# Optimization experiments

Measured on AMD Instinct MI355X. Metric: run time of the kernel, lower is better.

The kernel has to match this reference:

```python
import jax, jax.numpy as jnp
import numpy as np

N_HEADS = 16
HEAD_SIZE = 64
EMBED = 1024
BLOCK = 2048
B, T = 2, 2048


def setup_inputs() -> dict:
    key = jax.random.key(0)
    ks = jax.random.split(key, 6)
    scale = 0.02
    inputs = jax.random.normal(ks[0], (B, T, EMBED), dtype=jnp.float32)
    # per-head projection weights, stacked: [H, E, D]
    Wk = jax.random.normal(ks[1], (N_HEADS, EMBED, HEAD_SIZE), dtype=jnp.float32) * scale
    Wq = jax.random.normal(ks[2], (N_HEADS, EMBED, HEAD_SIZE), dtype=jnp.float32) * scale
    Wv = jax.random.normal(ks[3], (N_HEADS, EMBED, HEAD_SIZE), dtype=jnp.float32) * scale
    Wo = jax.random.normal(ks[4], (EMBED, EMBED), dtype=jnp.float32) * scale
    bo = jax.random.normal(ks[5], (EMBED,), dtype=jnp.float32) * scale
    return {"inputs": inputs, "Wk": Wk, "Wq": Wq, "Wv": Wv, "Wo": Wo, "bo": bo}


def reference(inputs, Wk, Wq, Wv, Wo, bo):
    # per-head projections: [B,H,T,D]
    k = jnp.einsum("bte,hed->bhtd", inputs, Wk)
    q = jnp.einsum("bte,hed->bhtd", inputs, Wq)
    v = jnp.einsum("bte,hed->bhtd", inputs, Wv)
    # NOTE: original computes wei = K @ Q^T (faithful reproduction)
    wei = jnp.einsum("bhtd,bhsd->bhts", k, q) * (HEAD_SIZE ** -0.5)
    causal = jnp.tril(jnp.ones((T, T), dtype=bool))  # tril==0 masked
    wei = jnp.where(causal, wei, -jnp.inf)
    wei = jax.nn.softmax(wei, axis=-1)
    out = jnp.einsum("bhts,bhsd->bhtd", wei, v)
    # concat heads along feature dim: [B,T,H*D]
    z = out.transpose(0, 2, 1, 3).reshape(B, T, N_HEADS * HEAD_SIZE)
    z = z @ Wo.T + bo  # match torch Linear(x) = x @ W^T + b
    return z
```

## Files before the change

kernel.cpp:

```cpp
#include <hip/hip_runtime.h>
#include <cstdint>
#include <cstddef>

typedef __bf16 bf8_t __attribute__((ext_vector_type(8)));
typedef float  f4_t  __attribute__((ext_vector_type(4)));

static __device__ __forceinline__ f4_t mfma16(bf8_t a, bf8_t b, f4_t c) {
    return __builtin_amdgcn_mfma_f32_16x16x32_bf16(a, b, c, 0, 0, 0);
}

#if defined(__has_builtin) && __has_builtin(__builtin_amdgcn_exp2f)
#define EXP2F(x) __builtin_amdgcn_exp2f(x)
#else
#define EXP2F(x) exp2f(x)
#endif

static __device__ __forceinline__ void async_ld16(const __bf16* g, __bf16* l) {
    __builtin_amdgcn_global_load_lds(
        (const __attribute__((address_space(1))) void*)(uintptr_t)g,
        (__attribute__((address_space(3))) void*)(uintptr_t)l, 16, 0, 0);
}


__global__ void __launch_bounds__(256) prep_all(const float* __restrict__ X,
                                                const float* __restrict__ Wo,
                                                const float* __restrict__ Wq,
                                                const float* __restrict__ Wk,
                                                const float* __restrict__ Wv,
                                                __bf16* __restrict__ Xbf,
                                                __bf16* __restrict__ Wobf,
                                                __bf16* __restrict__ Wqt,
                                                __bf16* __restrict__ Wkt,
                                                __bf16* __restrict__ Wvt) {
    __shared__ float tile[64][65];
    int bx = (int)blockIdx.x;
    if (bx < 2560) {
        const float* src; __bf16* dst; size_t base;
        if (bx < 2048) { src = X;  dst = Xbf;  base = (size_t)bx * 2048; }
        else           { src = Wo; dst = Wobf; base = (size_t)(bx - 2048) * 2048; }
        size_t i = base + (size_t)threadIdx.x * 8;
        float4 a = *(const float4*)(src + i);
        float4 b = *(const float4*)(src + i + 4);
        bf8_t o;
        o[0] = (__bf16)a.x; o[1] = (__bf16)a.y; o[2] = (__bf16)a.z; o[3] = (__bf16)a.w;
        o[4] = (__bf16)b.x; o[5] = (__bf16)b.y; o[6] = (__bf16)b.z; o[7] = (__bf16)b.w;
        *(bf8_t*)(dst + i) = o;
        return;
    }
    int wt = bx - 2560;
    int which = wt >> 8, inner = wt & 255;
    const float* W; __bf16* Wt;
    if (which == 0)      { W = Wq; Wt = Wqt; }
    else if (which == 1) { W = Wk; Wt = Wkt; }
    else                 { W = Wv; Wt = Wvt; }
    int h = inner >> 4, eb = inner & 15;
    int tx = threadIdx.x;
    int e = tx >> 2, dg = (tx & 3) * 16;
    const float* src = W + ((size_t)h * 1024 + eb * 64 + e) * 64 + dg;
#pragma unroll
    for (int i = 0; i < 4; ++i) {
        float4 v = *(const float4*)(src + i * 4);
        tile[dg + i * 4 + 0][e] = v.x;
        tile[dg + i * 4 + 1][e] = v.y;
        tile[dg + i * 4 + 2][e] = v.z;
        tile[dg + i * 4 + 3][e] = v.w;
    }
    __syncthreads();
    int d = tx >> 2, eg = (tx & 3) * 16;
    __bf16* dst = Wt + (size_t)(h * 64 + d) * 1024 + eb * 64 + eg;
    bf8_t o0, o1;
#pragma unroll
    for (int i = 0; i < 8; ++i) o0[i] = (__bf16)tile[d][eg + i];
#pragma unroll
    for (int i = 0; i < 8; ++i) o1[i] = (__bf16)tile[d][eg + 8 + i];
    *(bf8_t*)dst       = o0;
    *(bf8_t*)(dst + 8) = o1;
}

static __device__ __forceinline__ void gemm_tile128(const __bf16* __restrict__ A,
                                                    const __bf16* __restrict__ Bt,
                                                    __bf16* As, __bf16* Bs,
                                                    int m0, int n0, f4_t acc[4][4]) {
    const int tid  = threadIdx.x;
    const int lane = tid & 63;
    const int wv   = tid >> 6;
    const int lrow = lane >> 3;
    const int lsc  = lane & 7;
    const int quad = lane >> 4;
    const int l15  = lane & 15;
    const int wm = (wv & 1) * 64;
    const int wn = (wv >> 1) * 64;
    f4_t zero = {0.f, 0.f, 0.f, 0.f};
#pragma unroll
    for (int mi = 0; mi < 4; ++mi)
#pragma unroll
        for (int ni = 0; ni < 4; ++ni) acc[mi][ni] = zero;

    for (int kb = 0; kb < 16; ++kb) {
#pragma unroll
        for (int j = 0; j < 4; ++j) {
            int row = wv * 32 + j * 8 + lrow;
            int lc  = lsc ^ (row & 7);
            async_ld16(A + (size_t)(m0 + row) * 1024 + kb * 64 + lc * 8,
                       As + (wv * 32 + j * 8) * 64);
            async_ld16(Bt + (size_t)(n0 + row) * 1024 + kb * 64 + lc * 8,
                       Bs + (wv * 32 + j * 8) * 64);
        }
        __syncthreads();
#pragma unroll
        for (int ks = 0; ks < 2; ++ks) {
            bf8_t af[4], bfr[4];
#pragma unroll
            for (int mi = 0; mi < 4; ++mi) {
                int row = wm + mi * 16 + l15;
                int ch  = (ks * 4 + quad) ^ (row & 7);
                af[mi] = *(const bf8_t*)(As + row * 64 + ch * 8);
            }
#pragma unroll
            for (int ni = 0; ni < 4; ++ni) {
                int row = wn + ni * 16 + l15;
                int ch  = (ks * 4 + quad) ^ (row & 7);
                bfr[ni] = *(const bf8_t*)(Bs + row * 64 + ch * 8);
            }
#pragma unroll
            for (int mi = 0; mi < 4; ++mi)
#pragma unroll
                for (int ni = 0; ni < 4; ++ni)
                    acc[mi][ni] = mfma16(af[mi], bfr[ni], acc[mi][ni]);
        }
        __syncthreads();
    }
}

__global__ void __launch_bounds__(256, 3) gemm_proj(const __bf16* __restrict__ Xbf,
                                                    const __bf16* __restrict__ Wqt,
                                                    const __bf16* __restrict__ Wkt,
                                                    const __bf16* __restrict__ Wvt,
                                                    __bf16* __restrict__ Qb,
                                                    __bf16* __restrict__ Kb,
                                                    __bf16* __restrict__ Vt) {
    __shared__ __bf16 smem[17408];
    __bf16* As = smem;
    __bf16* Bs = smem + 8192;
    int which = blockIdx.y;
    const __bf16* Bt = which == 0 ? Wqt : (which == 1 ? Wkt : Wvt);
    int m0 = ((int)blockIdx.x >> 3) * 128;
    int n0 = ((int)blockIdx.x & 7) * 128;
    f4_t acc[4][4];
    gemm_tile128(Xbf, Bt, As, Bs, m0, n0, acc);
    const int lane = threadIdx.x & 63, wv = threadIdx.x >> 6;
    const int quad = lane >> 4, l15 = lane & 15;
    const int wm = (wv & 1) * 64, wn = (wv >> 1) * 64;
    const int STR = 136;
    if (which < 2) {
        __bf16* C = which ? Kb : Qb;
        const float scl = which ? 0.18033688f : 1.0f;
#pragma unroll
        for (int mi = 0; mi < 4; ++mi)
#pragma unroll
            for (int ni = 0; ni < 4; ++ni)
#pragma unroll
                for (int r = 0; r < 4; ++r) {
                    int ml = wm + mi * 16 + quad * 4 + r;
                    int nl = wn + ni * 16 + l15;
                    smem[ml * STR + nl] = (__bf16)(acc[mi][ni][r] * scl);
                }
        __syncthreads();
        int row = (int)threadIdx.x >> 1;
        int seg = (int)threadIdx.x & 1;
        int m = m0 + row;
        int b = m >> 11, t = m & 2047;
        int h = (n0 >> 6) + seg;
        __bf16* dst = C + ((size_t)(b * 16 + h) * 2048 + t) * 64;
        const __bf16* srcl = smem + row * STR + seg * 64;
#pragma unroll
        for (int k = 0; k < 8; ++k)
            *(bf8_t*)(dst + k * 8) = *(const bf8_t*)(srcl + k * 8);
    } else {
#pragma unroll
        for (int mi = 0; mi < 4; ++mi)
#pragma unroll
            for (int ni = 0; ni < 4; ++ni)
#pragma unroll
                for (int r = 0; r < 4; ++r) {
                    int ml = wm + mi * 16 + quad * 4 + r;
                    int nl = wn + ni * 16 + l15;
                    smem[nl * STR + ml] = (__bf16)acc[mi][ni][r];
                }
        __syncthreads();
        int b = m0 >> 11, tg0 = m0 & 2047;
        int nl = (int)threadIdx.x >> 1;
        int tc = ((int)threadIdx.x & 1) * 64;
        int n = n0 + nl, h = n >> 6, d = n & 63;
        __bf16* dst = Vt + ((size_t)(b * 16 + h) * 64 + d) * 2048 + tg0 + tc;
        const __bf16* srcl = smem + nl * STR + tc;
#pragma unroll
        for (int k = 0; k < 8; ++k)
            *(bf8_t*)(dst + k * 8) = *(const bf8_t*)(srcl + k * 8);
    }
}

static __device__ __forceinline__ void gemm_tile(const __bf16* __restrict__ A,
                                                 const __bf16* __restrict__ Bt,
                                                 __bf16* As, __bf16* Bs,
                                                 int m0, int n0, f4_t acc[4][2]) {
    const int tid  = threadIdx.x;
    const int lane = tid & 63;
    const int wv   = tid >> 6;
    const int lrow = lane >> 3;
    const int lsc  = lane & 7;
    const int quad = lane >> 4;
    const int l15  = lane & 15;
    const int wm = (wv & 1) * 64;
    const int wn = (wv >> 1) * 32;
    f4_t zero = {0.f, 0.f, 0.f, 0.f};
#pragma unroll
    for (int mi = 0; mi < 4; ++mi)
#pragma unroll
        for (int ni = 0; ni < 2; ++ni) acc[mi][ni] = zero;

    for (int kb = 0; kb < 16; ++kb) {
#pragma unroll
        for (int j = 0; j < 4; ++j) {
            int row = wv * 32 + j * 8 + lrow;
            int lc  = lsc ^ (row & 7);
            async_ld16(A + (size_t)(m0 + row) * 1024 + kb * 64 + lc * 8,
                       As + (wv * 32 + j * 8) * 64);
        }
#pragma unroll
        for (int j = 0; j < 2; ++j) {
            int row = wv * 16 + j * 8 + lrow;
            int lc  = lsc ^ (row & 7);
            async_ld16(Bt + (size_t)(n0 + row) * 1024 + kb * 64 + lc * 8,
                       Bs + (wv * 16 + j * 8) * 64);
        }
        __syncthreads();
#pragma unroll
        for (int ks = 0; ks < 2; ++ks) {
            bf8_t af[4], bfr[2];
#pragma unroll
            for (int mi = 0; mi < 4; ++mi) {
                int row = wm + mi * 16 + l15;
                int ch  = (ks * 4 + quad) ^ (row & 7);
                af[mi] = *(const bf8_t*)(As + row * 64 + ch * 8);
            }
#pragma unroll
            for (int ni = 0; ni < 2; ++ni) {
                int row = wn + ni * 16 + l15;
                int ch  = (ks * 4 + quad) ^ (row & 7);
                bfr[ni] = *(const bf8_t*)(Bs + row * 64 + ch * 8);
            }
#pragma unroll
            for (int mi = 0; mi < 4; ++mi)
#pragma unroll
                for (int ni = 0; ni < 2; ++ni)
                    acc[mi][ni] = mfma16(af[mi], bfr[ni], acc[mi][ni]);
        }
        __syncthreads();
    }
}

__global__ void __launch_bounds__(256) gemm_out(const __bf16* __restrict__ Ob,
                                                const __bf16* __restrict__ Wobf,
                                                const float* __restrict__ bo,
                                                float* __restrict__ out) {
    __shared__ __bf16 smem[128 * 64 + 64 * 64];
    __bf16* As = smem;
    __bf16* Bs = smem + 128 * 64;
    int m0 = ((int)blockIdx.x >> 4) * 128;
    int n0 = ((int)blockIdx.x & 15) * 64;
    f4_t acc[4][2];
    gemm_tile(Ob, Wobf, As, Bs, m0, n0, acc);
    const int lane = threadIdx.x & 63, wv = threadIdx.x >> 6;
    const int quad = lane >> 4, l15 = lane & 15;
    const int wm = (wv & 1) * 64, wn = (wv >> 1) * 32;
#pragma unroll
    for (int mi = 0; mi < 4; ++mi)
#pragma unroll
        for (int ni = 0; ni < 2; ++ni)
#pragma unroll
            for (int r = 0; r < 4; ++r) {
                int m = m0 + wm + mi * 16 + quad * 4 + r;
                int n = n0 + wn + ni * 16 + l15;
                out[(size_t)m * 1024 + n] = acc[mi][ni][r] + bo[n];
            }
}

__global__ void __launch_bounds__(256, 3) attn(const __bf16* __restrict__ Kb,
                                               const __bf16* __restrict__ Qb,
                                               const __bf16* __restrict__ Vt,
                                               __bf16* __restrict__ Ob,
                                               int* __restrict__ ctrs) {
    __shared__ __bf16 Qs[2][64 * 64];
    __shared__ __bf16 Vs[2][64 * 64];
    __shared__ __bf16 Ps[4][16 * 72];
    __shared__ int item_lds;
    const int tid = threadIdx.x, lane = tid & 63, wv = tid >> 6;
    const int quad = lane >> 4, l15 = lane & 15;
    const int lrow8 = lane >> 3, lchunk = lane & 7;
    int xcc;
    asm volatile("s_getreg_b32 %0, hwreg(HW_REG_XCC_ID)" : "=s"(xcc));
    xcc &= 7;
    int* ctr = ctrs + xcc * 16;
    __bf16* Psw = &Ps[wv][0];
    f4_t zero = {0.f, 0.f, 0.f, 0.f};

    for (;;) {
        if (tid == 0) item_lds = atomicAdd(ctr, 1);
        __syncthreads();
        const int q = item_lds;
        if (q >= 128) break;
        const int tt = 31 - (q >> 2);
        const int bh = xcc * 4 + (q & 3);
        const int b = bh >> 4, h = bh & 15;
        const int t0 = tt * 64;
        const int tw = t0 + wv * 16;
        const __bf16* Kp = Kb + (size_t)bh * 2048 * 64;
        const __bf16* Qp = Qb + (size_t)bh * 2048 * 64;
        const __bf16* Vp = Vt + (size_t)bh * 64 * 2048;

        bf8_t kfrag[2];
#pragma unroll
        for (int ks = 0; ks < 2; ++ks)
            kfrag[ks] = *(const bf8_t*)(Kp + (size_t)(tw + l15) * 64 + ks * 32 + quad * 8);

        f4_t oacc[4];
#pragma unroll
        for (int ni = 0; ni < 4; ++ni) oacc[ni] = zero;
        float lsum[4] = {0.f, 0.f, 0.f, 0.f};

        auto stage = [&](int buf, int s0) {
#pragma unroll
            for (int j = 0; j < 2; ++j) {
                int row = wv * 8 + j * 32 + lrow8;
                int cg  = lchunk ^ (row & 7);
                async_ld16(Qp + (size_t)(s0 + row) * 64 + cg * 8,
                           &Qs[buf][(wv * 8 + j * 32) * 64]);
                async_ld16(Vp + (size_t)row * 2048 + s0 + cg * 8,
                           &Vs[buf][(wv * 8 + j * 32) * 64]);
            }
        };

        const int nsb = tt + 1;
        stage(0, 0);
        for (int sb = 0; sb < nsb; ++sb) {
            const int cur = sb & 1;
            const int s0 = sb * 64;
            const bool masked = (sb == nsb - 1);
            __syncthreads();
            if (sb + 1 < nsb) stage(1 ^ cur, s0 + 64);
            const __bf16* Qc = &Qs[cur][0];
            const __bf16* Vc = &Vs[cur][0];
            f4_t sacc[4] = {zero, zero, zero, zero};
#pragma unroll
            for (int ks = 0; ks < 2; ++ks) {
                bf8_t qf[4];
#pragma unroll
                for (int st = 0; st < 4; ++st) {
                    int row = st * 16 + l15;
                    int ch  = (ks * 4 + quad) ^ (row & 7);
                    qf[st] = *(const bf8_t*)(Qc + row * 64 + ch * 8);
                }
#pragma unroll
                for (int st = 0; st < 4; ++st)
                    sacc[st] = mfma16(kfrag[ks], qf[st], sacc[st]);
            }
#pragma unroll
            for (int st = 0; st < 4; ++st)
#pragma unroll
                for (int r = 0; r < 4; ++r) {
                    float e = EXP2F(sacc[st][r]);
                    if (masked && (s0 + st * 16 + l15 > tw + quad * 4 + r)) e = 0.0f;
                    lsum[r] += e;
                    Psw[(quad * 4 + r) * 72 + st * 16 + l15] = (__bf16)e;
                }
            asm volatile("s_waitcnt lgkmcnt(0)" ::: "memory");
            bf8_t pf[2];
#pragma unroll
            for (int ks = 0; ks < 2; ++ks)
                pf[ks] = *(const bf8_t*)(Psw + l15 * 72 + ks * 32 + quad * 8);
#pragma unroll
            for (int ks = 0; ks < 2; ++ks) {
                bf8_t vf[4];
#pragma unroll
                for (int ni = 0; ni < 4; ++ni) {
                    int row = ni * 16 + l15;
                    int ch  = (ks * 4 + quad) ^ (row & 7);
                    vf[ni] = *(const bf8_t*)(Vc + row * 64 + ch * 8);
                }
#pragma unroll
                for (int ni = 0; ni < 4; ++ni)
                    oacc[ni] = mfma16(pf[ks], vf[ni], oacc[ni]);
            }
        }

#pragma unroll
        for (int r = 0; r < 4; ++r) {
            float l = lsum[r];
            l += __shfl_xor(l, 1);
            l += __shfl_xor(l, 2);
            l += __shfl_xor(l, 4);
            l += __shfl_xor(l, 8);
            float inv = 1.0f / l;
            int t = tw + quad * 4 + r;
#pragma unroll
            for (int ni = 0; ni < 4; ++ni)
                Ob[((size_t)(b * 2048 + t) * 16 + h) * 64 + ni * 16 + l15] =
                    (__bf16)(oacc[ni][r] * inv);
        }
    }
}

extern "C" void kernel_launch(void* const* d_in, const int* in_sizes, int n_in,
                              void* d_out, int out_size, void* d_ws, size_t ws_size,
                              hipStream_t stream) {
    const float* X  = (const float*)d_in[0];
    const float* Wk = (const float*)d_in[1];
    const float* Wq = (const float*)d_in[2];
    const float* Wv = (const float*)d_in[3];
    const float* Wo = (const float*)d_in[4];
    const float* bo = (const float*)d_in[5];
    float* out = (float*)d_out;

    __bf16* ws   = (__bf16*)d_ws;
    __bf16* Xbf  = ws;
    __bf16* Wqt  = ws + 4194304;
    __bf16* Wkt  = ws + 5242880;
    __bf16* Wvt  = ws + 6291456;
    __bf16* Wobf = ws + 7340032;
    __bf16* Qb   = ws + 8388608;
    __bf16* Kb   = ws + 12582912;
    __bf16* Vt   = ws + 16777216;
    __bf16* Ob   = ws + 20971520;
    int* ctrs = (int*)d_ws;

    prep_all<<<3328, 256, 0, stream>>>(X, Wo, Wq, Wk, Wv, Xbf, Wobf, Wqt, Wkt, Wvt);
    gemm_proj<<<dim3(256, 3), 256, 0, stream>>>(Xbf, Wqt, Wkt, Wvt, Qb, Kb, Vt);
    hipMemsetAsync(ctrs, 0, 512, stream);
    attn<<<768, 256, 0, stream>>>(Kb, Qb, Vt, Ob, ctrs);
    gemm_out<<<512, 256, 0, stream>>>(Ob, Wobf, bo, out);
}
```

Before: 174.7 us.

## Keep attention P in registers via lane permutes, raise occupancy, drop memset

The attention kernel swaps the QK MFMA operand order so the S tile comes out transposed, then builds the PV A-operand in registers using permlane32 swaps and xor shuffles instead of writing P to LDS and reading it back. This removes the per-wave P shared buffer and the LDS round trip, and collapses the row-sum to one scalar per lane. Launch bounds rise to 4 blocks per CU with 1024 persistent blocks, s_setprio is raised around the MFMA sections, and the counter reset moves from a separate memset into the prep kernel, using the output buffer for the counters. The extra cross-lane permutes add VALU work, and reusing the output as counter storage relies on gemm_out overwriting it afterward.

After: 173.2 us. No clear change (-0.9%).

```diff
diff --git a/kernel.cpp b/kernel.cpp
--- a/kernel.cpp
+++ b/kernel.cpp
@@ -4,6 +4,7 @@
 
 typedef __bf16 bf8_t __attribute__((ext_vector_type(8)));
 typedef float  f4_t  __attribute__((ext_vector_type(4)));
+typedef unsigned u32x2_t __attribute__((ext_vector_type(2)));
 
 static __device__ __forceinline__ f4_t mfma16(bf8_t a, bf8_t b, f4_t c) {
     return __builtin_amdgcn_mfma_f32_16x16x32_bf16(a, b, c, 0, 0, 0);
@@ -14,6 +15,27 @@
 #else
 #define EXP2F(x) exp2f(x)
 #endif
+
+static __device__ __forceinline__ void plane32swap(unsigned& a, unsigned& b) {
+#if defined(__has_builtin) && __has_builtin(__builtin_amdgcn_permlane32_swap)
+    u32x2_t r = __builtin_amdgcn_permlane32_swap(a, b, false, false);
+    a = r[0]; b = r[1];
+#else
+    unsigned ax = __shfl_xor(a, 32);
+    unsigned bx = __shfl_xor(b, 32);
+    bool hi = ((threadIdx.x & 63) >= 32);
+    unsigned na = hi ? bx : a;
+    unsigned nb = hi ? b : ax;
+    a = na; b = nb;
+#endif
+}
+
+static __device__ __forceinline__ unsigned pack2(float a, float b) {
+    __bf16 lo = (__bf16)a, hi = (__bf16)b;
+    unsigned short ulo = __builtin_bit_cast(unsigned short, lo);
+    unsigned short uhi = __builtin_bit_cast(unsigned short, hi);
+    return (unsigned)ulo | ((unsigned)uhi << 16);
+}
 
 static __device__ __forceinline__ void async_ld16(const __bf16* g, __bf16* l) {
     __builtin_amdgcn_global_load_lds(
@@ -31,9 +53,11 @@
                                                 __bf16* __restrict__ Wobf,
                                                 __bf16* __restrict__ Wqt,
                                                 __bf16* __restrict__ Wkt,
-                                                __bf16* __restrict__ Wvt) {
+                                                __bf16* __restrict__ Wvt,
+                                                int* __restrict__ ctrs) {
     __shared__ float tile[64][65];
     int bx = (int)blockIdx.x;
+    if (bx == 0 && threadIdx.x < 128) ctrs[threadIdx.x] = 0;
     if (bx < 2560) {
         const float* src; __bf16* dst; size_t base;
         if (bx < 2048) { src = X;  dst = Xbf;  base = (size_t)bx * 2048; }
@@ -286,23 +310,22 @@
             }
 }
 
-__global__ void __launch_bounds__(256, 3) attn(const __bf16* __restrict__ Kb,
+__global__ void __launch_bounds__(256, 4) attn(const __bf16* __restrict__ Kb,
                                                const __bf16* __restrict__ Qb,
                                                const __bf16* __restrict__ Vt,
                                                __bf16* __restrict__ Ob,
                                                int* __restrict__ ctrs) {
     __shared__ __bf16 Qs[2][64 * 64];
     __shared__ __bf16 Vs[2][64 * 64];
-    __shared__ __bf16 Ps[4][16 * 72];
     __shared__ int item_lds;
     const int tid = threadIdx.x, lane = tid & 63, wv = tid >> 6;
     const int quad = lane >> 4, l15 = lane & 15;
     const int lrow8 = lane >> 3, lchunk = lane & 7;
+    const bool qodd = (quad & 1) != 0;
     int xcc;
     asm volatile("s_getreg_b32 %0, hwreg(HW_REG_XCC_ID)" : "=s"(xcc));
     xcc &= 7;
     int* ctr = ctrs + xcc * 16;
-    __bf16* Psw = &Ps[wv][0];
     f4_t zero = {0.f, 0.f, 0.f, 0.f};
 
     for (;;) {
@@ -327,7 +350,7 @@
         f4_t oacc[4];
 #pragma unroll
         for (int ni = 0; ni < 4; ++ni) oacc[ni] = zero;
-        float lsum[4] = {0.f, 0.f, 0.f, 0.f};
+        float lsum = 0.f;
 
         auto stage = [&](int buf, int s0) {
 #pragma unroll
@@ -352,6 +375,7 @@
             const __bf16* Qc = &Qs[cur][0];
             const __bf16* Vc = &Vs[cur][0];
             f4_t sacc[4] = {zero, zero, zero, zero};
+            __builtin_amdgcn_s_setprio(1);
 #pragma unroll
             for (int ks = 0; ks < 2; ++ks) {
                 bf8_t qf[4];
@@ -363,22 +387,50 @@
                 }
 #pragma unroll
                 for (int st = 0; st < 4; ++st)
-                    sacc[st] = mfma16(kfrag[ks], qf[st], sacc[st]);
-            }
+                    sacc[st] = mfma16(qf[st], kfrag[ks], sacc[st]);
+            }
+            __builtin_amdgcn_s_setprio(0);
+            const int lim = tw + l15 - s0;
 #pragma unroll
             for (int st = 0; st < 4; ++st)
 #pragma unroll
                 for (int r = 0; r < 4; ++r) {
                     float e = EXP2F(sacc[st][r]);
-                    if (masked && (s0 + st * 16 + l15 > tw + quad * 4 + r)) e = 0.0f;
-                    lsum[r] += e;
-                    Psw[(quad * 4 + r) * 72 + st * 16 + l15] = (__bf16)e;
-                }
-            asm volatile("s_waitcnt lgkmcnt(0)" ::: "memory");
+                    if (masked && (st * 16 + quad * 4 + r > lim)) e = 0.0f;
+                    lsum += e;
+                    sacc[st][r] = e;
+                }
+            unsigned pk[4][2];
+#pragma unroll
+            for (int st = 0; st < 4; ++st)
+#pragma unroll
+                for (int rp = 0; rp < 2; ++rp)
+                    pk[st][rp] = pack2(sacc[st][2 * rp], sacc[st][2 * rp + 1]);
             bf8_t pf[2];
 #pragma unroll
-            for (int ks = 0; ks < 2; ++ks)
-                pf[ks] = *(const bf8_t*)(Psw + l15 * 72 + ks * 32 + quad * 8);
+            for (int ks = 0; ks < 2; ++ks) {
+                unsigned w0, w1, w2, w3;
+                {
+                    unsigned A = pk[2 * ks][0], B = pk[2 * ks + 1][0];
+                    plane32swap(A, B);
+                    unsigned As_ = __shfl_xor(A, 16);
+                    unsigned Bs_ = __shfl_xor(B, 16);
+                    w0 = qodd ? Bs_ : A;
+                    w2 = qodd ? B : As_;
+                }
+                {
+                    unsigned A = pk[2 * ks][1], B = pk[2 * ks + 1][1];
+                    plane32swap(A, B);
+                    unsigned As_ = __shfl_xor(A, 16);
+                    unsigned Bs_ = __shfl_xor(B, 16);
+                    w1 = qodd ? Bs_ : A;
+                    w3 = qodd ? B : As_;
+                }
+                union { unsigned u[4]; bf8_t v; } cv;
+                cv.u[0] = w0; cv.u[1] = w1; cv.u[2] = w2; cv.u[3] = w3;
+                pf[ks] = cv.v;
+            }
+            __builtin_amdgcn_s_setprio(1);
 #pragma unroll
             for (int ks = 0; ks < 2; ++ks) {
                 bf8_t vf[4];
@@ -392,21 +444,21 @@
                 for (int ni = 0; ni < 4; ++ni)
                     oacc[ni] = mfma16(pf[ks], vf[ni], oacc[ni]);
             }
-        }
-
+            __builtin_amdgcn_s_setprio(0);
+        }
+
+        float l = lsum;
+        l += __shfl_xor(l, 16);
+        l += __shfl_xor(l, 32);
+        float inv = 1.0f / l;
 #pragma unroll
         for (int r = 0; r < 4; ++r) {
-            float l = lsum[r];
-            l += __shfl_xor(l, 1);
-            l += __shfl_xor(l, 2);
-            l += __shfl_xor(l, 4);
-            l += __shfl_xor(l, 8);
-            float inv = 1.0f / l;
+            float invr = __shfl(inv, quad * 4 + r);
             int t = tw + quad * 4 + r;
 #pragma unroll
             for (int ni = 0; ni < 4; ++ni)
                 Ob[((size_t)(b * 2048 + t) * 16 + h) * 64 + ni * 16 + l15] =
-                    (__bf16)(oacc[ni][r] * inv);
+                    (__bf16)(oacc[ni][r] * invr);
         }
     }
 }
@@ -432,11 +484,10 @@
     __bf16* Kb   = ws + 12582912;
     __bf16* Vt   = ws + 16777216;
     __bf16* Ob   = ws + 20971520;
-    int* ctrs = (int*)d_ws;
-
-    prep_all<<<3328, 256, 0, stream>>>(X, Wo, Wq, Wk, Wv, Xbf, Wobf, Wqt, Wkt, Wvt);
+    int* ctrs = (int*)out;
+
+    prep_all<<<3328, 256, 0, stream>>>(X, Wo, Wq, Wk, Wv, Xbf, Wobf, Wqt, Wkt, Wvt, ctrs);
     gemm_proj<<<dim3(256, 3), 256, 0, stream>>>(Xbf, Wqt, Wkt, Wvt, Qb, Kb, Vt);
-    hipMemsetAsync(ctrs, 0, 512, stream);
-    attn<<<768, 256, 0, stream>>>(Kb, Qb, Vt, Ob, ctrs);
+    attn<<<1024, 256, 0, stream>>>(Kb, Qb, Vt, Ob, ctrs);
     gemm_out<<<512, 256, 0, stream>>>(Ob, Wobf, bo, out);
 }
```
